# Kernel optimization log

Hardware: AMD Instinct MI355X
Metric: run time of the kernel (lower is better)

## Reference

```python
import jax, jax.numpy as jnp
import numpy as np
from functools import partial

NUM_GROUP = 512   # S
GROUP_SIZE = 32   # K
BN_EPS = 1e-5
STD_EPS = 1e-5


def fps(xyz, n_samples):
    # xyz: [N,3] -> indices [n_samples] (farthest point sampling, start at idx 0)
    N = xyz.shape[0]
    def body(carry, _):
        dists, last = carry
        d = jnp.sum((xyz - xyz[last]) ** 2, axis=-1)
        dists = jnp.minimum(dists, d)
        nxt = jnp.argmax(dists).astype(jnp.int32)
        return (dists, nxt), last
    init = (jnp.full((N,), jnp.inf, xyz.dtype), jnp.array(0, jnp.int32))
    _, idx = jax.lax.scan(body, init, None, length=n_samples)
    return idx


def knn_idx(xyz, center, k):
    # xyz [N,3], center [S,3] -> k nearest neighbor indices [S,k]
    d2 = (jnp.sum(center ** 2, -1)[:, None] + jnp.sum(xyz ** 2, -1)[None, :]
          - 2.0 * center @ xyz.T)
    _, idx = jax.lax.top_k(-d2, k)
    return idx


def conv1(x, W, b):
    # 1x1 Conv1d: x [M,Cin,L], W [Cout,Cin] -> [M,Cout,L]
    return jnp.einsum('oc,mcl->mol', W, x) + b[None, :, None]


def bn(x, g, b):
    # BatchNorm1d eval mode with running_mean=0, running_var=1
    scale = g / jnp.sqrt(1.0 + BN_EPS)
    return x * scale[None, :, None] + b[None, :, None]


def res_block(x, W1, b1, g1, bb1, W2, b2, g2, bb2):
    # ConvBNReLURes1D, res_expansion=1.0
    h = jax.nn.relu(bn(conv1(x, W1, b1), g1, bb1))
    h = bn(conv1(h, W2, b2), g2, bb2)
    return jax.nn.relu(h + x)


def reference(xyz, alpha, beta, Wt, bt, gt, bbt,
              Wpre1, bpre1, gpre1, bbpre1, Wpre2, bpre2, gpre2, bbpre2,
              Wpos1, bpos1, gpos1, bbpos1, Wpos2, bpos2, gpos2, bbpos2):
    B, N, _ = xyz.shape
    S, K = NUM_GROUP, GROUP_SIZE
    C = Wt.shape[0]

    # ---- LocalGrouper: FPS + KNN + gather + normalize ----
    c_idx = jax.vmap(partial(fps, n_samples=S))(xyz)          # [B,S]
    center = jax.vmap(lambda p, i: p[i])(xyz, c_idx)          # [B,S,3]
    n_idx = jax.vmap(partial(knn_idx, k=K))(xyz, center)      # [B,S,K]
    nbr = jax.vmap(lambda p, i: p[i])(xyz, n_idx)             # [B,S,K,3]

    mean = center[:, :, None, :]
    diff = nbr - mean
    std = jnp.std(diff.reshape(B, -1), axis=-1, ddof=1).reshape(B, 1, 1, 1)
    nbr = alpha * (diff / (std + STD_EPS)) + beta
    grouped = jnp.concatenate(
        [nbr, jnp.broadcast_to(mean, (B, S, K, 3))], axis=-1)  # [B,S,K,6]

    # ---- Extraction ----
    x = grouped.transpose(0, 1, 3, 2).reshape(B * S, 6, K)     # [B*S,6,K]
    h = jax.nn.relu(bn(conv1(x, Wt, bt), gt, bbt))             # [B*S,C,K]
    h = res_block(h, Wpre1, bpre1, gpre1, bbpre1, Wpre2, bpre2, gpre2, bbpre2)
    pooled = jnp.max(h, axis=-1)                               # [B*S,C]
    feat = pooled.reshape(B, S, C).transpose(0, 2, 1)          # [B,C,S]
    feat = res_block(feat, Wpos1, bpos1, gpos1, bbpos1, Wpos2, bpos2, gpos2, bbpos2)
    return feat.transpose(0, 2, 1)                             # [B,S,C]


def setup_inputs() -> dict:
    key = jax.random.key(0)
    ks = jax.random.split(key, 12)
    B, N, C = 8, 8192, 384
    s6 = 1.0 / np.sqrt(6.0)
    sc = 1.0 / np.sqrt(C)
    return {
        'xyz': jax.random.normal(ks[0], (B, N, 3), jnp.float32),
        'alpha': jnp.ones((1, 1, 1, 3), jnp.float32),
        'beta': jnp.zeros((1, 1, 1, 3), jnp.float32),
        'Wt': jax.random.normal(ks[1], (C, 6), jnp.float32) * s6,
        'bt': jax.random.normal(ks[2], (C,), jnp.float32) * 0.02,
        'gt': jnp.ones((C,), jnp.float32), 'bbt': jnp.zeros((C,), jnp.float32),
        'Wpre1': jax.random.normal(ks[3], (C, C), jnp.float32) * sc,
        'bpre1': jax.random.normal(ks[4], (C,), jnp.float32) * 0.02,
        'gpre1': jnp.ones((C,), jnp.float32), 'bbpre1': jnp.zeros((C,), jnp.float32),
        'Wpre2': jax.random.normal(ks[5], (C, C), jnp.float32) * sc,
        'bpre2': jax.random.normal(ks[6], (C,), jnp.float32) * 0.02,
        'gpre2': jnp.ones((C,), jnp.float32), 'bbpre2': jnp.zeros((C,), jnp.float32),
        'Wpos1': jax.random.normal(ks[7], (C, C), jnp.float32) * sc,
        'bpos1': jax.random.normal(ks[8], (C,), jnp.float32) * 0.02,
        'gpos1': jnp.ones((C,), jnp.float32), 'bbpos1': jnp.zeros((C,), jnp.float32),
        'Wpos2': jax.random.normal(ks[9], (C, C), jnp.float32) * sc,
        'bpos2': jax.random.normal(ks[10], (C,), jnp.float32) * 0.02,
        'gpos2': jnp.ones((C,), jnp.float32), 'bbpos2': jnp.zeros((C,), jnp.float32),
    }
```

## Files before the change

kernel.cpp:

```cpp
#include <hip/hip_runtime.h>
#include <hip/hip_bf16.h>
#include <math.h>

typedef __bf16 bf16x8 __attribute__((ext_vector_type(8)));
typedef float f32x4 __attribute__((ext_vector_type(4)));

#define NPTS 8192
#define SGRP 512
#define KNBR 32
#define CCH 384
#define LDSP 392

static __device__ __forceinline__ unsigned short f2b(float f) {
  union { float f; unsigned u; } v; v.f = f;
  return (unsigned short)((v.u + 0x7fffu + ((v.u >> 16) & 1u)) >> 16);
}
static __device__ __forceinline__ float b2f(unsigned short u) {
  union { unsigned u; float f; } v; v.u = ((unsigned)u) << 16;
  return v.f;
}
static __device__ __forceinline__ unsigned pk2(float a, float b) {
  return (unsigned)f2b(a) | ((unsigned)f2b(b) << 16);
}

#define DPPMAX(v, ctrl) \
  fmaxf((v), __int_as_float(__builtin_amdgcn_update_dpp(0, __float_as_int(v), (ctrl), 0xf, 0xf, false)))

struct FoldArgs {
  const float *W, *b, *g, *bb;
  unsigned short* Wd;
  float* bd;
};
__global__ void fold4_bf16(FoldArgs a0, FoldArgs a1, FoldArgs a2, FoldArgs a3) {
  FoldArgs a = (blockIdx.y == 0) ? a0 : (blockIdx.y == 1) ? a1 : (blockIdx.y == 2) ? a2 : a3;
  int o = blockIdx.x;
  float sc = a.g[o] / sqrtf(1.0f + 1e-5f);
  for (int c = threadIdx.x; c < CCH; c += blockDim.x)
    a.Wd[o * CCH + c] = f2b(a.W[o * CCH + c] * sc);
  if (threadIdx.x == 0) a.bd[o] = a.b[o] * sc + a.bb[o];
}
__global__ void fold_w_f32(const float* __restrict__ W, const float* __restrict__ b,
                           const float* __restrict__ g, const float* __restrict__ bb,
                           float* __restrict__ Wd, float* __restrict__ bd, int Cin) {
  int o = blockIdx.x;
  float sc = g[o] / sqrtf(1.0f + 1e-5f);
  for (int c = threadIdx.x; c < Cin; c += blockDim.x)
    Wd[o * Cin + c] = W[o * Cin + c] * sc;
  if (threadIdx.x == 0) bd[o] = b[o] * sc + bb[o];
}

__global__ __launch_bounds__(512) void fps_kernel(const float* __restrict__ xyz,
                                                  int* __restrict__ cIdx) {
  #pragma clang fp contract(off)
  __shared__ float xs[NPTS], ys[NPTS], zs[NPTS];
  __shared__ uint2 slots[2][8];
  const int b = blockIdx.x, tid = threadIdx.x;
  const int lane = tid & 63, wid = tid >> 6;
  const float* xb = xyz + (size_t)b * NPTS * 3;

  float X[16], Y[16], Z[16], D[16];
  {
    const float4* src = (const float4*)xb + tid * 12;
    float tmp[48];
    #pragma unroll
    for (int q = 0; q < 12; ++q) {
      float4 t = src[q];
      tmp[q * 4 + 0] = t.x; tmp[q * 4 + 1] = t.y;
      tmp[q * 4 + 2] = t.z; tmp[q * 4 + 3] = t.w;
    }
    #pragma unroll
    for (int j = 0; j < 16; ++j) {
      X[j] = tmp[j * 3 + 0]; Y[j] = tmp[j * 3 + 1]; Z[j] = tmp[j * 3 + 2];
      D[j] = __builtin_inff();
      int p = tid * 16 + j;
      xs[p] = X[j]; ys[p] = Y[j]; zs[p] = Z[j];
    }
  }
  if (tid == 0) cIdx[b * SGRP] = 0;
  __syncthreads();
  float cx = xs[0], cy = ys[0], cz = zs[0];

  for (int step = 1; step < SGRP; ++step) {
    float bv = -1.0f; int bi = 0;
    #pragma unroll
    for (int j = 0; j < 16; ++j) {
      float dx = X[j] - cx, dy = Y[j] - cy, dz = Z[j] - cz;
      float d = (dx * dx + dy * dy) + dz * dz;
      float nd = fminf(D[j], d);
      D[j] = nd;
      if (nd > bv) { bv = nd; bi = tid * 16 + j; }
    }
    float m = bv;
    m = DPPMAX(m, 0x111);
    m = DPPMAX(m, 0x112);
    m = DPPMAX(m, 0x114);
    m = DPPMAX(m, 0x118);
    m = DPPMAX(m, 0x142);
    m = DPPMAX(m, 0x143);
    float wmax = __uint_as_float(__builtin_amdgcn_readlane(__float_as_uint(m), 63));
    unsigned long long msk = __ballot(bv == wmax);
    int srcLane = (int)__builtin_ctzll(msk);
    int wbi = __builtin_amdgcn_readlane(bi, srcLane);
    const int par = step & 1;
    if (lane == 0) slots[par][wid] = make_uint2(__float_as_uint(wmax), (unsigned)wbi);
    __syncthreads();
    float gbv = -1.0f; int gi = 0;
    #pragma unroll
    for (int w = 0; w < 8; ++w) {
      uint2 s = slots[par][w];
      float fv = __uint_as_float(s.x);
      if (fv > gbv) { gbv = fv; gi = (int)s.y; }
    }
    if (tid == 0) cIdx[b * SGRP + step] = gi;
    cx = xs[gi]; cy = ys[gi]; cz = zs[gi];
  }
}

__global__ __launch_bounds__(256) void knn_kernel(const float* __restrict__ xyz,
                                                  const int* __restrict__ cIdx,
                                                  float* __restrict__ nbrDiff,
                                                  float* __restrict__ ctrW,
                                                  float* __restrict__ partials) {
  #pragma clang fp contract(off)
  __shared__ unsigned long long keyBuf[4];
  __shared__ int winners[KNBR];
  const int cid = blockIdx.x;
  const int b = cid >> 9;
  const int tid = threadIdx.x;
  const float* xb = xyz + (size_t)b * NPTS * 3;
  const int cI = cIdx[cid];
  const float cx = xb[cI * 3], cy = xb[cI * 3 + 1], cz = xb[cI * 3 + 2];
  const float cs = (cx * cx + cy * cy) + cz * cz;

  float d2[32];
  float mv = __builtin_inff(); int mi = 0;
  #pragma unroll
  for (int j = 0; j < 32; ++j) {
    int p = tid + (j << 8);
    float x = xb[p * 3], y = xb[p * 3 + 1], z = xb[p * 3 + 2];
    float ps = (x * x + y * y) + z * z;
    float dot = (cx * x + cy * y) + cz * z;
    d2[j] = (cs + ps) - 2.0f * dot;
    if (d2[j] < mv) { mv = d2[j]; mi = p; }
  }
  if (tid < 4) keyBuf[tid] = 0xFFFFFFFFFFFFFFFFull;
  __syncthreads();

  for (int it = 0; it < KNBR; ++it) {
    if (tid == 0) keyBuf[(it + 2) & 3] = 0xFFFFFFFFFFFFFFFFull;
    float bv = mv; int bi = mi;
    #pragma unroll
    for (int s = 1; s < 64; s <<= 1) {
      float ov = __shfl_xor(bv, s); int oi = __shfl_xor(bi, s);
      if (ov < bv || (ov == bv && oi < bi)) { bv = ov; bi = oi; }
    }
    if ((tid & 63) == 0) {
      unsigned u = __float_as_uint(bv);
      unsigned m = u ^ (unsigned)(((int)u >> 31) | 0x80000000);
      unsigned long long key = (((unsigned long long)m) << 32) | (unsigned long long)bi;
      atomicMin(&keyBuf[it & 3], key);
    }
    __syncthreads();
    unsigned long long k = keyBuf[it & 3];
    int wi = (int)(k & 0x1FFFu);
    if (tid == 0) winners[it] = wi;
    if (tid == (wi & 255)) {
      #pragma unroll
      for (int j = 0; j < 32; ++j)
        if (wi == tid + (j << 8)) d2[j] = __builtin_inff();
      mv = __builtin_inff(); mi = 0;
      #pragma unroll
      for (int j = 0; j < 32; ++j)
        if (d2[j] < mv) { mv = d2[j]; mi = tid + (j << 8); }
    }
  }
  __syncthreads();

  float sum = 0.f, sq = 0.f;
  if (tid < KNBR) {
    int w = winners[tid];
    float dx = xb[w * 3] - cx, dy = xb[w * 3 + 1] - cy, dz = xb[w * 3 + 2] - cz;
    size_t o = ((size_t)cid * KNBR + tid) * 3;
    nbrDiff[o + 0] = dx; nbrDiff[o + 1] = dy; nbrDiff[o + 2] = dz;
    sum = (dx + dy) + dz;
    sq = (dx * dx + dy * dy) + dz * dz;
  }
  if (tid < 64) {
    #pragma unroll
    for (int s = 1; s < 64; s <<= 1) { sum += __shfl_xor(sum, s); sq += __shfl_xor(sq, s); }
    if (tid == 0) { partials[cid * 2] = sum; partials[cid * 2 + 1] = sq; }
  }
  if (tid < 3) ctrW[(size_t)cid * 3 + tid] = xb[cI * 3 + tid];
}

__global__ __launch_bounds__(256) void std_kernel(const float* __restrict__ partials,
                                                  float* __restrict__ stdv) {
  __shared__ double sd[256], sq[256];
  const int b = blockIdx.x, t = threadIdx.x;
  int i0 = (b * 512 + t) * 2;
  sd[t] = (double)partials[i0] + (double)partials[i0 + 512];
  sq[t] = (double)partials[i0 + 1] + (double)partials[i0 + 513];
  for (int st = 128; st > 0; st >>= 1) {
    __syncthreads();
    if (t < st) { sd[t] += sd[t + st]; sq[t] += sq[t + st]; }
  }
  if (t == 0) {
    double n = (double)(SGRP * KNBR * 3);
    double mean = sd[0] / n;
    double var = (sq[0] - sd[0] * mean) / (n - 1.0);
    stdv[b] = (float)sqrt(var);
  }
}

static __device__ __forceinline__ void gemm_half(const unsigned short* __restrict__ W,
                                                 const unsigned short* ht,
                                                 int oBase, int n0, int r16, int g4,
                                                 f32x4 acc[3][4]) {
  for (int ks = 0; ks < 12; ++ks) {
    const int kOff = ks * 32 + g4 * 8;
    bf16x8 a[3], bb[4];
    #pragma unroll
    for (int i = 0; i < 3; ++i)
      a[i] = *(const bf16x8*)(W + (size_t)(oBase + i * 16 + r16) * CCH + kOff);
    #pragma unroll
    for (int j = 0; j < 4; ++j)
      bb[j] = *(const bf16x8*)(ht + (n0 + j * 16 + r16) * LDSP + kOff);
    #pragma unroll
    for (int i = 0; i < 3; ++i) {
      #pragma unroll
      for (int j = 0; j < 4; ++j)
        acc[i][j] = __builtin_amdgcn_mfma_f32_16x16x32_bf16(a[i], bb[j], acc[i][j], 0, 0, 0);
    }
  }
}

__global__ __launch_bounds__(512) void group_mlp_kernel(
    const float* __restrict__ alpha, const float* __restrict__ beta,
    const float* __restrict__ WtF, const float* __restrict__ btF,
    const unsigned short* __restrict__ W1, const float* __restrict__ b1,
    const unsigned short* __restrict__ W2, const float* __restrict__ b2,
    const float* __restrict__ nbrDiff, const float* __restrict__ ctrW,
    const float* __restrict__ stdv, unsigned short* __restrict__ feat) {
  __shared__ unsigned short ht[128 * LDSP];
  __shared__ float xtw[128 * 8];
  __shared__ float wtl[CCH * 6];
  __shared__ float btl[CCH];

  const int tid = threadIdx.x;
  const int lane = tid & 63, wid = tid >> 6;
  const int r16 = lane & 15, g4 = lane >> 4;
  const int bid = blockIdx.x;
  const int b = bid >> 7;
  const int sBase = (bid & 127) << 2;

  for (int i = tid; i < CCH * 6; i += 512) wtl[i] = WtF[i];
  for (int i = tid; i < CCH; i += 512) btl[i] = btF[i];

  const float inv = 1.0f / (stdv[b] + 1e-5f);
  if (tid < 128) {
    int g = tid >> 5, kk = tid & 31;
    int cid = b * SGRP + sBase + g;
    const float* nb = nbrDiff + ((size_t)cid * KNBR + kk) * 3;
    const float* cc = ctrW + (size_t)cid * 3;
    #pragma unroll
    for (int c = 0; c < 3; ++c) {
      xtw[tid * 8 + c] = alpha[c] * (nb[c] * inv) + beta[c];
      xtw[tid * 8 + 3 + c] = cc[c];
    }
  }
  __syncthreads();

  {
    int l = tid & 127, oi = tid >> 7;
    float xv[6];
    #pragma unroll
    for (int c = 0; c < 6; ++c) xv[c] = xtw[l * 8 + c];
    for (int j = 0; j < 96; ++j) {
      int o = oi * 96 + j;
      float v = btl[o];
      #pragma unroll
      for (int c = 0; c < 6; ++c) v += wtl[o * 6 + c] * xv[c];
      ht[l * LDSP + o] = f2b(fmaxf(v, 0.0f));
    }
  }
  __syncthreads();

  const int oBase = wid * 48;

  for (int half = 0; half < 2; ++half) {
    const int n0 = half * 64;
    f32x4 acc[3][4];
    #pragma unroll
    for (int i = 0; i < 3; ++i) {
      #pragma unroll
      for (int j = 0; j < 4; ++j) acc[i][j] = (f32x4){0.f, 0.f, 0.f, 0.f};
    }
    gemm_half(W1, ht, oBase, n0, r16, g4, acc);
    __syncthreads();
    #pragma unroll
    for (int i = 0; i < 3; ++i) {
      int o4 = oBase + i * 16 + g4 * 4;
      float bs0 = b1[o4], bs1 = b1[o4 + 1], bs2 = b1[o4 + 2], bs3 = b1[o4 + 3];
      #pragma unroll
      for (int j = 0; j < 4; ++j) {
        int row = n0 + j * 16 + r16;
        unsigned u0 = pk2(fmaxf(acc[i][j][0] + bs0, 0.f), fmaxf(acc[i][j][1] + bs1, 0.f));
        unsigned u1 = pk2(fmaxf(acc[i][j][2] + bs2, 0.f), fmaxf(acc[i][j][3] + bs3, 0.f));
        *(uint2*)(ht + row * LDSP + o4) = make_uint2(u0, u1);
      }
    }
    __syncthreads();
  }

  for (int half = 0; half < 2; ++half) {
    const int n0 = half * 64;
    f32x4 acc[3][4];
    #pragma unroll
    for (int i = 0; i < 3; ++i) {
      #pragma unroll
      for (int j = 0; j < 4; ++j) acc[i][j] = (f32x4){0.f, 0.f, 0.f, 0.f};
    }
    gemm_half(W2, ht, oBase, n0, r16, g4, acc);

    float bias2[3][4];
    #pragma unroll
    for (int i = 0; i < 3; ++i) {
      int o4 = oBase + i * 16 + g4 * 4;
      #pragma unroll
      for (int r = 0; r < 4; ++r) bias2[i][r] = b2[o4 + r];
    }
    float mx[3][2][4];
    #pragma unroll
    for (int i = 0; i < 3; ++i) {
      #pragma unroll
      for (int gg = 0; gg < 2; ++gg) {
        #pragma unroll
        for (int r = 0; r < 4; ++r) mx[i][gg][r] = 0.f;
      }
    }
    #pragma unroll
    for (int j = 0; j < 4; ++j) {
      int l = n0 + j * 16 + r16;
      float xv[6];
      #pragma unroll
      for (int c = 0; c < 6; ++c) xv[c] = xtw[l * 8 + c];
      #pragma unroll
      for (int i = 0; i < 3; ++i) {
        int o4 = oBase + i * 16 + g4 * 4;
        #pragma unroll
        for (int r = 0; r < 4; ++r) {
          float h0 = btl[o4 + r];
          #pragma unroll
          for (int c = 0; c < 6; ++c) h0 += wtl[(o4 + r) * 6 + c] * xv[c];
          h0 = fmaxf(h0, 0.f);
          float v = fmaxf(acc[i][j][r] + bias2[i][r] + h0, 0.f);
          mx[i][j >> 1][r] = fmaxf(mx[i][j >> 1][r], v);
        }
      }
    }
    #pragma unroll
    for (int i = 0; i < 3; ++i) {
      #pragma unroll
      for (int gg = 0; gg < 2; ++gg) {
        float m0 = mx[i][gg][0], m1 = mx[i][gg][1], m2 = mx[i][gg][2], m3 = mx[i][gg][3];
        #pragma unroll
        for (int s = 1; s < 16; s <<= 1) {
          m0 = fmaxf(m0, __shfl_xor(m0, s));
          m1 = fmaxf(m1, __shfl_xor(m1, s));
          m2 = fmaxf(m2, __shfl_xor(m2, s));
          m3 = fmaxf(m3, __shfl_xor(m3, s));
        }
        if (r16 == 0) {
          int sIdx = sBase + half * 2 + gg;
          size_t fi = ((size_t)(b * SGRP + sIdx)) * CCH + oBase + i * 16 + g4 * 4;
          *(uint2*)(feat + fi) = make_uint2(pk2(m0, m1), pk2(m2, m3));
        }
      }
    }
  }
}

__global__ __launch_bounds__(256) void pos_kernel(const unsigned short* __restrict__ feat,
                                                  const unsigned short* __restrict__ Wp1,
                                                  const float* __restrict__ bp1,
                                                  const unsigned short* __restrict__ Wp2,
                                                  const float* __restrict__ bp2,
                                                  float* __restrict__ out) {
  __shared__ unsigned short h1[16 * LDSP];
  const int tid = threadIdx.x;
  const int lane = tid & 63, wid = tid >> 6;
  const int r16 = lane & 15, g4 = lane >> 4;
  const int bid = blockIdx.x;
  const int b = bid >> 5;
  const int s0 = (bid & 31) << 4;
  const size_t rowBase = ((size_t)(b * SGRP + s0 + r16)) * CCH;

  f32x4 acc[6];
  #pragma unroll
  for (int i = 0; i < 6; ++i) acc[i] = (f32x4){0.f, 0.f, 0.f, 0.f};
  for (int ks = 0; ks < 12; ++ks) {
    const int kOff = ks * 32 + g4 * 8;
    bf16x8 bfr = *(const bf16x8*)(feat + rowBase + kOff);
    #pragma unroll
    for (int i = 0; i < 6; ++i) {
      bf16x8 a = *(const bf16x8*)(Wp1 + (size_t)(wid * 96 + i * 16 + r16) * CCH + kOff);
      acc[i] = __builtin_amdgcn_mfma_f32_16x16x32_bf16(a, bfr, acc[i], 0, 0, 0);
    }
  }
  #pragma unroll
  for (int i = 0; i < 6; ++i) {
    int o4 = wid * 96 + i * 16 + g4 * 4;
    unsigned u0 = pk2(fmaxf(acc[i][0] + bp1[o4 + 0], 0.f), fmaxf(acc[i][1] + bp1[o4 + 1], 0.f));
    unsigned u1 = pk2(fmaxf(acc[i][2] + bp1[o4 + 2], 0.f), fmaxf(acc[i][3] + bp1[o4 + 3], 0.f));
    *(uint2*)(h1 + r16 * LDSP + o4) = make_uint2(u0, u1);
  }
  __syncthreads();

  f32x4 acc2[6];
  #pragma unroll
  for (int i = 0; i < 6; ++i) acc2[i] = (f32x4){0.f, 0.f, 0.f, 0.f};
  for (int ks = 0; ks < 12; ++ks) {
    const int kOff = ks * 32 + g4 * 8;
    bf16x8 bfr = *(const bf16x8*)(h1 + r16 * LDSP + kOff);
    #pragma unroll
    for (int i = 0; i < 6; ++i) {
      bf16x8 a = *(const bf16x8*)(Wp2 + (size_t)(wid * 96 + i * 16 + r16) * CCH + kOff);
      acc2[i] = __builtin_amdgcn_mfma_f32_16x16x32_bf16(a, bfr, acc2[i], 0, 0, 0);
    }
  }
  #pragma unroll
  for (int i = 0; i < 6; ++i) {
    int o4 = wid * 96 + i * 16 + g4 * 4;
    uint2 rr = *(const uint2*)(feat + rowBase + o4);
    float4 v;
    v.x = fmaxf(acc2[i][0] + bp2[o4 + 0] + b2f((unsigned short)(rr.x & 0xffff)), 0.f);
    v.y = fmaxf(acc2[i][1] + bp2[o4 + 1] + b2f((unsigned short)(rr.x >> 16)), 0.f);
    v.z = fmaxf(acc2[i][2] + bp2[o4 + 2] + b2f((unsigned short)(rr.y & 0xffff)), 0.f);
    v.w = fmaxf(acc2[i][3] + bp2[o4 + 3] + b2f((unsigned short)(rr.y >> 16)), 0.f);
    *(float4*)(out + rowBase + o4) = v;
  }
}

extern "C" void kernel_launch(void* const* d_in, const int* in_sizes, int n_in,
                              void* d_out, int out_size, void* d_ws, size_t ws_size,
                              hipStream_t stream) {
  (void)in_sizes; (void)n_in; (void)out_size; (void)ws_size;
  const float* xyz   = (const float*)d_in[0];
  const float* alpha = (const float*)d_in[1];
  const float* beta  = (const float*)d_in[2];
  const float* Wt    = (const float*)d_in[3];
  const float* bt    = (const float*)d_in[4];
  const float* gt    = (const float*)d_in[5];
  const float* bbt   = (const float*)d_in[6];
  const float* Wpre1 = (const float*)d_in[7];
  const float* bpre1 = (const float*)d_in[8];
  const float* gpre1 = (const float*)d_in[9];
  const float* bbpre1= (const float*)d_in[10];
  const float* Wpre2 = (const float*)d_in[11];
  const float* bpre2 = (const float*)d_in[12];
  const float* gpre2 = (const float*)d_in[13];
  const float* bbpre2= (const float*)d_in[14];
  const float* Wpos1 = (const float*)d_in[15];
  const float* bpos1 = (const float*)d_in[16];
  const float* gpos1 = (const float*)d_in[17];
  const float* bbpos1= (const float*)d_in[18];
  const float* Wpos2 = (const float*)d_in[19];
  const float* bpos2 = (const float*)d_in[20];
  const float* gpos2 = (const float*)d_in[21];
  const float* bbpos2= (const float*)d_in[22];

  char* ws = (char*)d_ws;
  size_t off = 0;
  auto alloc = [&](size_t bytes) -> void* {
    void* p = ws + off;
    off += (bytes + 255) & ~(size_t)255;
    return p;
  };
  float* WtF = (float*)alloc(CCH * 6 * 4);
  float* btF = (float*)alloc(CCH * 4);
  unsigned short* W1 = (unsigned short*)alloc(CCH * CCH * 2);
  float* b1 = (float*)alloc(CCH * 4);
  unsigned short* W2 = (unsigned short*)alloc(CCH * CCH * 2);
  float* b2 = (float*)alloc(CCH * 4);
  unsigned short* Wp1 = (unsigned short*)alloc(CCH * CCH * 2);
  float* bp1 = (float*)alloc(CCH * 4);
  unsigned short* Wp2 = (unsigned short*)alloc(CCH * CCH * 2);
  float* bp2 = (float*)alloc(CCH * 4);
  int* cIdx = (int*)alloc(8 * SGRP * 4);
  float* ctrW = (float*)alloc(8 * SGRP * 3 * 4);
  float* nbrD = (float*)alloc((size_t)8 * SGRP * KNBR * 3 * 4);
  float* partials = (float*)alloc(8 * SGRP * 2 * 4);
  float* stdv = (float*)alloc(8 * 4);
  unsigned short* feat = (unsigned short*)alloc((size_t)8 * SGRP * CCH * 2);

  fold_w_f32<<<CCH, 64, 0, stream>>>(Wt, bt, gt, bbt, WtF, btF, 6);
  FoldArgs fa0{Wpre1, bpre1, gpre1, bbpre1, W1, b1};
  FoldArgs fa1{Wpre2, bpre2, gpre2, bbpre2, W2, b2};
  FoldArgs fa2{Wpos1, bpos1, gpos1, bbpos1, Wp1, bp1};
  FoldArgs fa3{Wpos2, bpos2, gpos2, bbpos2, Wp2, bp2};
  fold4_bf16<<<dim3(CCH, 4), 128, 0, stream>>>(fa0, fa1, fa2, fa3);

  fps_kernel<<<8, 512, 0, stream>>>(xyz, cIdx);
  knn_kernel<<<8 * SGRP, 256, 0, stream>>>(xyz, cIdx, nbrD, ctrW, partials);
  std_kernel<<<8, 256, 0, stream>>>(partials, stdv);
  group_mlp_kernel<<<1024, 512, 0, stream>>>(alpha, beta, WtF, btF, W1, b1, W2, b2,
                                             nbrD, ctrW, stdv, feat);
  pos_kernel<<<256, 256, 0, stream>>>(feat, Wp1, bp1, Wp2, bp2, (float*)d_out);
}
```

Before: 1.076 ms.

## Split FPS across four cooperating blocks per batch with global-memory barrier exchange

```diff
diff --git a/kernel.cpp b/kernel.cpp
--- a/kernel.cpp
+++ b/kernel.cpp
@@ -49,46 +49,47 @@
   if (threadIdx.x == 0) bd[o] = b[o] * sc + bb[o];
 }
 
-__global__ __launch_bounds__(512) void fps_kernel(const float* __restrict__ xyz,
-                                                  int* __restrict__ cIdx) {
+__global__ __launch_bounds__(256) void fps_kernel(const float* __restrict__ xyz,
+                                                  int* __restrict__ cIdx,
+                                                  unsigned long long* __restrict__ pub) {
   #pragma clang fp contract(off)
-  __shared__ float xs[NPTS], ys[NPTS], zs[NPTS];
-  __shared__ uint2 slots[2][8];
-  const int b = blockIdx.x, tid = threadIdx.x;
-  const int lane = tid & 63, wid = tid >> 6;
+  __shared__ uint4 slotA[2][4];
+  __shared__ unsigned slotB[2][4];
+  const int tid = threadIdx.x, lane = tid & 63, wid = tid >> 6;
+  const int blk = blockIdx.x;
+  const int b = blk >> 2, w = blk & 3;
   const float* xb = xyz + (size_t)b * NPTS * 3;
-
-  float X[16], Y[16], Z[16], D[16];
+  const int base = w * 2048;
+
+  float X[8], Y[8], Z[8], D[8];
   {
-    const float4* src = (const float4*)xb + tid * 12;
-    float tmp[48];
-    #pragma unroll
-    for (int q = 0; q < 12; ++q) {
+    const float4* src = (const float4*)(xb + (size_t)base * 3) + tid * 6;
+    float tmp[24];
+    #pragma unroll
+    for (int q = 0; q < 6; ++q) {
       float4 t = src[q];
       tmp[q * 4 + 0] = t.x; tmp[q * 4 + 1] = t.y;
       tmp[q * 4 + 2] = t.z; tmp[q * 4 + 3] = t.w;
     }
     #pragma unroll
-    for (int j = 0; j < 16; ++j) {
+    for (int j = 0; j < 8; ++j) {
       X[j] = tmp[j * 3 + 0]; Y[j] = tmp[j * 3 + 1]; Z[j] = tmp[j * 3 + 2];
       D[j] = __builtin_inff();
-      int p = tid * 16 + j;
-      xs[p] = X[j]; ys[p] = Y[j]; zs[p] = Z[j];
-    }
-  }
-  if (tid == 0) cIdx[b * SGRP] = 0;
-  __syncthreads();
-  float cx = xs[0], cy = ys[0], cz = zs[0];
+    }
+  }
+  if (w == 0 && tid == 0) cIdx[b * SGRP] = 0;
+  float cx = xb[0], cy = xb[1], cz = xb[2];
 
   for (int step = 1; step < SGRP; ++step) {
-    float bv = -1.0f; int bi = 0;
-    #pragma unroll
-    for (int j = 0; j < 16; ++j) {
+    const int par = step & 1;
+    float bv = -1.0f; int bi = 0; float bx = 0.f, by = 0.f, bz = 0.f;
+    #pragma unroll
+    for (int j = 0; j < 8; ++j) {
       float dx = X[j] - cx, dy = Y[j] - cy, dz = Z[j] - cz;
       float d = (dx * dx + dy * dy) + dz * dz;
       float nd = fminf(D[j], d);
       D[j] = nd;
-      if (nd > bv) { bv = nd; bi = tid * 16 + j; }
+      if (nd > bv) { bv = nd; bi = base + tid * 8 + j; bx = X[j]; by = Y[j]; bz = Z[j]; }
     }
     float m = bv;
     m = DPPMAX(m, 0x111);
@@ -100,19 +101,50 @@
     float wmax = __uint_as_float(__builtin_amdgcn_readlane(__float_as_uint(m), 63));
     unsigned long long msk = __ballot(bv == wmax);
     int srcLane = (int)__builtin_ctzll(msk);
-    int wbi = __builtin_amdgcn_readlane(bi, srcLane);
-    const int par = step & 1;
-    if (lane == 0) slots[par][wid] = make_uint2(__float_as_uint(wmax), (unsigned)wbi);
+    unsigned wbi = (unsigned)__builtin_amdgcn_readlane(bi, srcLane);
+    unsigned wx = (unsigned)__builtin_amdgcn_readlane(__float_as_int(bx), srcLane);
+    unsigned wy = (unsigned)__builtin_amdgcn_readlane(__float_as_int(by), srcLane);
+    unsigned wz = (unsigned)__builtin_amdgcn_readlane(__float_as_int(bz), srcLane);
+    if (lane == 0) {
+      slotA[par][wid] = make_uint4(__float_as_uint(wmax), wbi, wx, wy);
+      slotB[par][wid] = wz;
+    }
     __syncthreads();
-    float gbv = -1.0f; int gi = 0;
-    #pragma unroll
-    for (int w = 0; w < 8; ++w) {
-      uint2 s = slots[par][w];
+    float kv = -1.0f; unsigned ki = 0, kx = 0, ky = 0, kz = 0;
+    #pragma unroll
+    for (int w4 = 0; w4 < 4; ++w4) {
+      uint4 s = slotA[par][w4];
       float fv = __uint_as_float(s.x);
-      if (fv > gbv) { gbv = fv; gi = (int)s.y; }
-    }
-    if (tid == 0) cIdx[b * SGRP + step] = gi;
-    cx = xs[gi]; cy = ys[gi]; cz = zs[gi];
+      if (fv > kv) { kv = fv; ki = s.y; kx = s.z; ky = s.w; kz = slotB[par][w4]; }
+    }
+    if (tid == 0) {
+      unsigned long long* P = pub + (((size_t)par * 8 + b) * 4 + w) * 3;
+      __hip_atomic_store(P + 0, (((unsigned long long)__float_as_uint(kv)) << 32) | ki,
+                         __ATOMIC_RELAXED, __HIP_MEMORY_SCOPE_AGENT);
+      __hip_atomic_store(P + 1, ((unsigned long long)kx) | (((unsigned long long)ky) << 32),
+                         __ATOMIC_RELAXED, __HIP_MEMORY_SCOPE_AGENT);
+      __hip_atomic_store(P + 2, ((unsigned long long)kz) | (((unsigned long long)(unsigned)step) << 32),
+                         __ATOMIC_RELEASE, __HIP_MEMORY_SCOPE_AGENT);
+    }
+    float gv = -1.0f; unsigned gi = 0; float nx = 0.f, ny = 0.f, nz = 0.f;
+    #pragma unroll 1
+    for (int pw = 0; pw < 4; ++pw) {
+      const unsigned long long* P = pub + (((size_t)par * 8 + b) * 4 + pw) * 3;
+      unsigned long long zsv;
+      do {
+        zsv = __hip_atomic_load(P + 2, __ATOMIC_ACQUIRE, __HIP_MEMORY_SCOPE_AGENT);
+      } while ((unsigned)(zsv >> 32) != (unsigned)step);
+      unsigned long long vi = __hip_atomic_load(P + 0, __ATOMIC_RELAXED, __HIP_MEMORY_SCOPE_AGENT);
+      unsigned long long xy = __hip_atomic_load(P + 1, __ATOMIC_RELAXED, __HIP_MEMORY_SCOPE_AGENT);
+      float fv = __uint_as_float((unsigned)(vi >> 32));
+      if (fv > gv) {
+        gv = fv; gi = (unsigned)vi;
+        nx = __uint_as_float((unsigned)xy); ny = __uint_as_float((unsigned)(xy >> 32));
+        nz = __uint_as_float((unsigned)zsv);
+      }
+    }
+    if (w == 0 && tid == 0) cIdx[b * SGRP + step] = (int)gi;
+    cx = nx; cy = ny; cz = nz;
   }
 }
 
@@ -492,6 +524,7 @@
   float* partials = (float*)alloc(8 * SGRP * 2 * 4);
   float* stdv = (float*)alloc(8 * 4);
   unsigned short* feat = (unsigned short*)alloc((size_t)8 * SGRP * CCH * 2);
+  unsigned long long* pub = (unsigned long long*)alloc(2 * 8 * 4 * 3 * 8);
 
   fold_w_f32<<<CCH, 64, 0, stream>>>(Wt, bt, gt, bbt, WtF, btF, 6);
   FoldArgs fa0{Wpre1, bpre1, gpre1, bbpre1, W1, b1};
@@ -500,7 +533,8 @@
   FoldArgs fa3{Wpos2, bpos2, gpos2, bbpos2, Wp2, bp2};
   fold4_bf16<<<dim3(CCH, 4), 128, 0, stream>>>(fa0, fa1, fa2, fa3);
 
-  fps_kernel<<<8, 512, 0, stream>>>(xyz, cIdx);
+  hipMemsetAsync(pub, 0, 2 * 8 * 4 * 3 * 8, stream);
+  fps_kernel<<<32, 256, 0, stream>>>(xyz, cIdx, pub);
   knn_kernel<<<8 * SGRP, 256, 0, stream>>>(xyz, cIdx, nbrD, ctrW, partials);
   std_kernel<<<8, 256, 0, stream>>>(partials, stdv);
   group_mlp_kernel<<<1024, 512, 0, stream>>>(alpha, beta, WtF, btF, W1, b1, W2, b2,
```

New measurement: 3.564 ms. 231% more time.

## Process two batches per FPS block and carry winner coordinates through reductions

Applied to the files above, without the earlier changes.

```diff
diff --git a/kernel.cpp b/kernel.cpp
--- a/kernel.cpp
+++ b/kernel.cpp
@@ -49,70 +49,120 @@
   if (threadIdx.x == 0) bd[o] = b[o] * sc + bb[o];
 }
 
-__global__ __launch_bounds__(512) void fps_kernel(const float* __restrict__ xyz,
-                                                  int* __restrict__ cIdx) {
+static __device__ __forceinline__ void fps_wave_reduce(
+    float (&X)[16], float (&Y)[16], float (&Z)[16], float (&D)[16],
+    float cx, float cy, float cz, int tid,
+    float &kv, unsigned &ki, unsigned &kx, unsigned &ky, unsigned &kz) {
   #pragma clang fp contract(off)
-  __shared__ float xs[NPTS], ys[NPTS], zs[NPTS];
-  __shared__ uint2 slots[2][8];
-  const int b = blockIdx.x, tid = threadIdx.x;
-  const int lane = tid & 63, wid = tid >> 6;
-  const float* xb = xyz + (size_t)b * NPTS * 3;
-
-  float X[16], Y[16], Z[16], D[16];
+  float bv = -1.0f; int bi = 0; float bx = 0.f, by = 0.f, bz = 0.f;
+  #pragma unroll
+  for (int j = 0; j < 16; ++j) {
+    float dx = X[j] - cx, dy = Y[j] - cy, dz = Z[j] - cz;
+    float d = (dx * dx + dy * dy) + dz * dz;
+    float nd = fminf(D[j], d);
+    D[j] = nd;
+    if (nd > bv) { bv = nd; bi = tid * 16 + j; bx = X[j]; by = Y[j]; bz = Z[j]; }
+  }
+  float m = bv;
+  m = DPPMAX(m, 0x111);
+  m = DPPMAX(m, 0x112);
+  m = DPPMAX(m, 0x114);
+  m = DPPMAX(m, 0x118);
+  m = DPPMAX(m, 0x142);
+  m = DPPMAX(m, 0x143);
+  float wmax = __uint_as_float(__builtin_amdgcn_readlane(__float_as_uint(m), 63));
+  unsigned long long msk = __ballot(bv == wmax);
+  int srcLane = (int)__builtin_ctzll(msk);
+  kv = wmax;
+  ki = (unsigned)__builtin_amdgcn_readlane(bi, srcLane);
+  kx = (unsigned)__builtin_amdgcn_readlane(__float_as_int(bx), srcLane);
+  ky = (unsigned)__builtin_amdgcn_readlane(__float_as_int(by), srcLane);
+  kz = (unsigned)__builtin_amdgcn_readlane(__float_as_int(bz), srcLane);
+}
+
+__global__ __launch_bounds__(512, 2) void fps_kernel(const float* __restrict__ xyz,
+                                                     int* __restrict__ cIdx) {
+  #pragma clang fp contract(off)
+  __shared__ uint4 slotA[2][16];
+  __shared__ unsigned slotZ[2][16];
+  const int tid = threadIdx.x, lane = tid & 63, wid = tid >> 6;
+  const int b0 = blockIdx.x * 2, b1 = b0 + 1;
+  const float* xA = xyz + (size_t)b0 * NPTS * 3;
+  const float* xB = xyz + (size_t)b1 * NPTS * 3;
+
+  float XA[16], YA[16], ZA[16], DA[16];
+  float XB[16], YB[16], ZB[16], DB[16];
   {
-    const float4* src = (const float4*)xb + tid * 12;
+    const float4* srcA = (const float4*)xA + tid * 12;
+    const float4* srcB = (const float4*)xB + tid * 12;
     float tmp[48];
     #pragma unroll
     for (int q = 0; q < 12; ++q) {
-      float4 t = src[q];
+      float4 t = srcA[q];
       tmp[q * 4 + 0] = t.x; tmp[q * 4 + 1] = t.y;
       tmp[q * 4 + 2] = t.z; tmp[q * 4 + 3] = t.w;
     }
     #pragma unroll
     for (int j = 0; j < 16; ++j) {
-      X[j] = tmp[j * 3 + 0]; Y[j] = tmp[j * 3 + 1]; Z[j] = tmp[j * 3 + 2];
-      D[j] = __builtin_inff();
-      int p = tid * 16 + j;
-      xs[p] = X[j]; ys[p] = Y[j]; zs[p] = Z[j];
-    }
-  }
-  if (tid == 0) cIdx[b * SGRP] = 0;
-  __syncthreads();
-  float cx = xs[0], cy = ys[0], cz = zs[0];
+      XA[j] = tmp[j * 3 + 0]; YA[j] = tmp[j * 3 + 1]; ZA[j] = tmp[j * 3 + 2];
+      DA[j] = __builtin_inff();
+    }
+    #pragma unroll
+    for (int q = 0; q < 12; ++q) {
+      float4 t = srcB[q];
+      tmp[q * 4 + 0] = t.x; tmp[q * 4 + 1] = t.y;
+      tmp[q * 4 + 2] = t.z; tmp[q * 4 + 3] = t.w;
+    }
+    #pragma unroll
+    for (int j = 0; j < 16; ++j) {
+      XB[j] = tmp[j * 3 + 0]; YB[j] = tmp[j * 3 + 1]; ZB[j] = tmp[j * 3 + 2];
+      DB[j] = __builtin_inff();
+    }
+  }
+  if (tid == 0) { cIdx[b0 * SGRP] = 0; cIdx[b1 * SGRP] = 0; }
+  float cxA = xA[0], cyA = xA[1], czA = xA[2];
+  float cxB = xB[0], cyB = xB[1], czB = xB[2];
 
   for (int step = 1; step < SGRP; ++step) {
-    float bv = -1.0f; int bi = 0;
-    #pragma unroll
-    for (int j = 0; j < 16; ++j) {
-      float dx = X[j] - cx, dy = Y[j] - cy, dz = Z[j] - cz;
-      float d = (dx * dx + dy * dy) + dz * dz;
-      float nd = fminf(D[j], d);
-      D[j] = nd;
-      if (nd > bv) { bv = nd; bi = tid * 16 + j; }
-    }
-    float m = bv;
-    m = DPPMAX(m, 0x111);
-    m = DPPMAX(m, 0x112);
-    m = DPPMAX(m, 0x114);
-    m = DPPMAX(m, 0x118);
-    m = DPPMAX(m, 0x142);
-    m = DPPMAX(m, 0x143);
-    float wmax = __uint_as_float(__builtin_amdgcn_readlane(__float_as_uint(m), 63));
-    unsigned long long msk = __ballot(bv == wmax);
-    int srcLane = (int)__builtin_ctzll(msk);
-    int wbi = __builtin_amdgcn_readlane(bi, srcLane);
     const int par = step & 1;
-    if (lane == 0) slots[par][wid] = make_uint2(__float_as_uint(wmax), (unsigned)wbi);
+    float kv; unsigned ki, kx, ky, kz;
+    fps_wave_reduce(XA, YA, ZA, DA, cxA, cyA, czA, tid, kv, ki, kx, ky, kz);
+    if (lane == 0) {
+      slotA[par][wid] = make_uint4(__float_as_uint(kv), ki, kx, ky);
+      slotZ[par][wid] = kz;
+    }
+    fps_wave_reduce(XB, YB, ZB, DB, cxB, cyB, czB, tid, kv, ki, kx, ky, kz);
+    if (lane == 0) {
+      slotA[par][8 + wid] = make_uint4(__float_as_uint(kv), ki, kx, ky);
+      slotZ[par][8 + wid] = kz;
+    }
     __syncthreads();
-    float gbv = -1.0f; int gi = 0;
+    float gvA = -1.0f; unsigned giA = 0;
     #pragma unroll
     for (int w = 0; w < 8; ++w) {
-      uint2 s = slots[par][w];
+      uint4 s = slotA[par][w];
       float fv = __uint_as_float(s.x);
-      if (fv > gbv) { gbv = fv; gi = (int)s.y; }
-    }
-    if (tid == 0) cIdx[b * SGRP + step] = gi;
-    cx = xs[gi]; cy = ys[gi]; cz = zs[gi];
+      if (fv > gvA) {
+        gvA = fv; giA = s.y;
+        cxA = __uint_as_float(s.z); cyA = __uint_as_float(s.w);
+        czA = __uint_as_float(slotZ[par][w]);
+      }
+    }
+    float gvB = -1.0f; unsigned giB = 0;
+    #pragma unroll
+    for (int w = 0; w < 8; ++w) {
+      uint4 s = slotA[par][8 + w];
+      float fv = __uint_as_float(s.x);
+      if (fv > gvB) {
+        gvB = fv; giB = s.y;
+        cxB = __uint_as_float(s.z); cyB = __uint_as_float(s.w);
+        czB = __uint_as_float(slotZ[par][8 + w]);
+      }
+    }
+    if (tid == 0) {
+      cIdx[b0 * SGRP + step] = (int)giA;
+      cIdx[b1 * SGRP + step] = (int)giB;
+    }
   }
 }
 
@@ -500,7 +550,7 @@
   FoldArgs fa3{Wpos2, bpos2, gpos2, bbpos2, Wp2, bp2};
   fold4_bf16<<<dim3(CCH, 4), 128, 0, stream>>>(fa0, fa1, fa2, fa3);
 
-  fps_kernel<<<8, 512, 0, stream>>>(xyz, cIdx);
+  fps_kernel<<<4, 512, 0, stream>>>(xyz, cIdx);
   knn_kernel<<<8 * SGRP, 256, 0, stream>>>(xyz, cIdx, nbrD, ctrW, partials);
   std_kernel<<<8, 256, 0, stream>>>(partials, stdv);
   group_mlp_kernel<<<1024, 512, 0, stream>>>(alpha, beta, WtF, btF, W1, b1, W2, b2,
```

After: 1.955 ms. +81.7%, slower.
